# Performance work log

Hardware: AMD Instinct MI355X
Metric: run time of the kernel (lower is better)

## Reference

```python
import jax, jax.numpy as jnp
import numpy as np

B, N, K = 2, 8192, 9
FEAT_C, COST_C, FLOW_C = 128, 64, 3
CH = [128, 128]          # PointConv output channels
MLP = [128, 64]          # pointwise Conv1d channels
WN = 16                  # WeightNet output width
HID = [8, 8]             # WeightNet hidden widths
SLOPE = 0.1              # leaky relu slope
EPS = 1e-5
CLAMP = (-200.0, 200.0)


def setup_inputs() -> dict:
    key = jax.random.key(0)
    ks = iter(jax.random.split(key, 64))
    def nrm(shape, s=0.02):
        return jax.random.normal(next(ks), shape, jnp.float32) * s
    inp = {}
    inp["xyz"] = jax.random.normal(next(ks), (B, N, 3), jnp.float32)
    inp["feats"] = jax.random.normal(next(ks), (B, FEAT_C, N), jnp.float32)
    inp["cost_volume"] = jax.random.normal(next(ks), (B, COST_C, N), jnp.float32)
    inp["flow"] = jax.random.normal(next(ks), (B, FLOW_C, N), jnp.float32)
    last = FEAT_C + COST_C + FLOW_C
    for i, co in enumerate(CH):
        cin = last + 3
        p = f"pc{i}_"
        inp[p + "w1"] = nrm((HID[0], 3)); inp[p + "b1"] = jnp.zeros((HID[0],), jnp.float32)
        inp[p + "w2"] = nrm((HID[1], HID[0])); inp[p + "b2"] = jnp.zeros((HID[1],), jnp.float32)
        inp[p + "w3"] = nrm((WN, HID[1])); inp[p + "b3"] = jnp.zeros((WN,), jnp.float32)
        inp[p + "linW"] = nrm((co, cin * WN)); inp[p + "linb"] = jnp.zeros((co,), jnp.float32)
        last = co
    for i, co in enumerate(MLP):
        inp[f"mlp{i}_W"] = nrm((co, last)); inp[f"mlp{i}_b"] = jnp.zeros((co,), jnp.float32)
        last = co
    inp["fc_W"] = nrm((3, last)); inp["fc_b"] = jnp.zeros((3,), jnp.float32)
    return inp


def _bn(x, axes):
    m = x.mean(axes, keepdims=True)
    v = x.var(axes, keepdims=True)
    return (x - m) / jnp.sqrt(v + EPS)


def _leaky(x):
    return jnp.where(x >= 0, x, SLOPE * x)


def _knn_idx(xyz, k):
    # xyz: [B,N,3] -> idx [B,N,K] of k nearest (incl. self)
    sq = jnp.sum(xyz * xyz, -1)                       # [B,N]
    d = sq[:, :, None] + sq[:, None, :] - 2.0 * jnp.einsum('bnc,bmc->bnm', xyz, xyz)
    return jax.lax.top_k(-d, k)[1]                    # [B,N,K]


def _gather(a, idx):
    # a: [B,N,C], idx: [B,N,K] -> [B,N,K,C]
    return jax.vmap(lambda x, i: x[i])(a, idx)


def _pointconv(xyz, points, idx, w1, b1, w2, b2, w3, b3, linW, linb):
    # xyz [B,N,3], points [B,C,N] -> [B,out,N]
    g_xyz = _gather(xyz, idx) - xyz[:, :, None, :]    # [B,N,K,3] relative coords
    g_pts = _gather(jnp.transpose(points, (0, 2, 1)), idx)  # [B,N,K,C]
    grouped = jnp.concatenate([g_pts, g_xyz], -1)     # [B,N,K,C+3]
    # WeightNet on relative coords: 3 -> 8 -> 8 -> 16 (bn+relu each)
    h = jax.nn.relu(_bn(g_xyz @ w1.T + b1, (0, 1, 2)))
    h = jax.nn.relu(_bn(h @ w2.T + b2, (0, 1, 2)))
    w = jax.nn.relu(_bn(h @ w3.T + b3, (0, 1, 2)))    # [B,N,K,WN]
    bsz, n = grouped.shape[0], grouped.shape[1]
    agg = jnp.einsum('bnkc,bnkw->bncw', grouped, w).reshape(bsz, n, -1)
    out = agg @ linW.T + linb                         # [B,N,out]
    out = _leaky(_bn(out, (0, 1)))
    return jnp.transpose(out, (0, 2, 1))              # [B,out,N]


def reference(xyz, feats, cost_volume, flow,
              pc0_w1, pc0_b1, pc0_w2, pc0_b2, pc0_w3, pc0_b3, pc0_linW, pc0_linb,
              pc1_w1, pc1_b1, pc1_w2, pc1_b2, pc1_w3, pc1_b3, pc1_linW, pc1_linb,
              mlp0_W, mlp0_b, mlp1_W, mlp1_b, fc_W, fc_b):
    idx = _knn_idx(xyz, K)
    x = jnp.concatenate([feats, cost_volume, flow], axis=1)  # [B, feat+cost+flow, N]
    x = _pointconv(xyz, x, idx, pc0_w1, pc0_b1, pc0_w2, pc0_b2, pc0_w3, pc0_b3, pc0_linW, pc0_linb)
    x = _pointconv(xyz, x, idx, pc1_w1, pc1_b1, pc1_w2, pc1_b2, pc1_w3, pc1_b3, pc1_linW, pc1_linb)
    x = _leaky(jnp.einsum('oc,bcn->bon', mlp0_W, x) + mlp0_b[None, :, None])
    x = _leaky(jnp.einsum('oc,bcn->bon', mlp1_W, x) + mlp1_b[None, :, None])
    fl = jnp.einsum('oc,bcn->bon', fc_W, x) + fc_b[None, :, None]
    return x, jnp.clip(fl, CLAMP[0], CLAMP[1])
```

## Files before the change

### kernel.cpp

```cpp
#include <hip/hip_runtime.h>

#define NBATCH 2
#define NPTS   8192
#define NPT    (NBATCH*NPTS)
#define KNN    9
#define SEG    16
#define SEGN   (NPTS/SEG)
#define SCAP   16
#define SSTR   17

typedef unsigned short u16;
typedef unsigned int   u32;
typedef short bf16x8 __attribute__((ext_vector_type(8)));
typedef float f32x4  __attribute__((ext_vector_type(4)));

__device__ __forceinline__ float wred(float v){
#pragma unroll
  for(int o=32;o>0;o>>=1) v += __shfl_down(v,o);
  return v;
}

__device__ __forceinline__ u16 f2b(float f){
  u32 u = __float_as_uint(f);
  return (u16)((u + 0x7fffu + ((u>>16)&1u)) >> 16);
}

__device__ __forceinline__ float bumpup(float x){
  u32 u = __float_as_uint(x);
  if(u == 0x80000000u) u = 1u;
  else if((int)u >= 0) u += 1u;
  else u -= 1u;
  return __uint_as_float(u);
}

__global__ __launch_bounds__(256) void k_build_xin(
    const float* __restrict__ feats, const float* __restrict__ cost,
    const float* __restrict__ flow, float* __restrict__ xin)
{
  __shared__ float buf[196][67];
  int t = threadIdx.x;
  int pt0 = blockIdx.x*64;
  int b = pt0 >> 13, n0 = pt0 & (NPTS-1);
  int lane = t & 63, grp = t >> 6;
  const float* f  = feats + (size_t)b*128*NPTS + n0 + lane;
  const float* cv = cost  + (size_t)b*64 *NPTS + n0 + lane;
  const float* fl = flow  + (size_t)b*3  *NPTS + n0 + lane;
  for(int c=grp; c<128; c+=4) buf[c][lane]      = f[(size_t)c*NPTS];
  for(int c=grp; c<64;  c+=4) buf[128+c][lane]  = cv[(size_t)c*NPTS];
  if(grp<3) buf[192+grp][lane] = fl[(size_t)grp*NPTS];
  else      buf[195][lane] = 0.f;
  __syncthreads();
  for(int e=t; e<64*49; e+=256){
    int p = e/49, q = e-p*49;
    float4 v = make_float4(buf[4*q][p], buf[4*q+1][p], buf[4*q+2][p], buf[4*q+3][p]);
    *(float4*)(xin + (size_t)(pt0+p)*196 + 4*q) = v;
  }
}

__global__ __launch_bounds__(256) void k_thr(
    const float* __restrict__ xyz, float* __restrict__ thr)
{
  __shared__ float md[4][64][9];
  int t = threadIdx.x, lane = t & 63, wave = t >> 6;
  int qb = blockIdx.x;
  int b = qb >> 7;
  int n = (qb & 127)*64 + lane;
  const float* xb = xyz + (size_t)b*NPTS*3;
  float qx=xb[3*n], qy=xb[3*n+1], qz=xb[3*n+2];
  float qs = __fadd_rn(__fadd_rn(__fmul_rn(qx,qx),__fmul_rn(qy,qy)),__fmul_rn(qz,qz));
  float bd[KNN];
#pragma unroll
  for(int i=0;i<KNN;i++) bd[i]=__builtin_inff();
  for(int i=0;i<128;i++){
    int m = (wave*128 + i)*16;
    float cx=xb[3*m], cy=xb[3*m+1], cz=xb[3*m+2];
    float s = __fadd_rn(__fadd_rn(__fmul_rn(cx,cx),__fmul_rn(cy,cy)),__fmul_rn(cz,cz));
    float dot = fmaf(cz,qz, fmaf(cy,qy, __fmul_rn(cx,qx)));
    float d = __fsub_rn(__fadd_rn(qs,s), __fmul_rn(2.0f,dot));
    if(d < bd[KNN-1]){
      bd[KNN-1]=d;
#pragma unroll
      for(int r=KNN-2;r>=0;r--){
        if(bd[r+1] < bd[r]){ float td=bd[r]; bd[r]=bd[r+1]; bd[r+1]=td; }
      }
    }
  }
#pragma unroll
  for(int i=0;i<KNN;i++) md[wave][lane][i]=bd[i];
  __syncthreads();
  if(t < 64){
    float b2[KNN];
#pragma unroll
    for(int i=0;i<KNN;i++) b2[i]=__builtin_inff();
    for(int w=0;w<4;w++){
#pragma unroll
      for(int i=0;i<KNN;i++){
        float d = md[w][t][i];
        if(d < b2[KNN-1]){
          b2[KNN-1]=d;
#pragma unroll
          for(int r=KNN-2;r>=0;r--){
            if(b2[r+1] < b2[r]){ float td=b2[r]; b2[r]=b2[r+1]; b2[r+1]=td; }
          }
        }
      }
    }
    thr[(b<<13) + (qb & 127)*64 + t] = b2[KNN-1];
  }
}

__global__ __launch_bounds__(256) void k_knn_part(
    const float* __restrict__ xyz, const float* __restrict__ thr,
    float* __restrict__ pd, int* __restrict__ pi)
{
  __shared__ float4 cbuf[256];
  __shared__ float sdq[256*SSTR];
  __shared__ int   sqi[256*SSTR];
  int t = threadIdx.x;
  int seg = blockIdx.x & (SEG-1);
  int qc  = blockIdx.x >> 4;
  int b = qc >> 5;
  int n = (qc & 31)*256 + t;
  int pt = (b<<13) + n;
  const float* xb = xyz + (size_t)b*NPTS*3;
  float qx=xb[3*n], qy=xb[3*n+1], qz=xb[3*n+2];
  float qs = __fadd_rn(__fadd_rn(__fmul_rn(qx,qx),__fmul_rn(qy,qy)),__fmul_rn(qz,qz));
  float init = bumpup(thr[pt]);
  float bd[KNN]; int bi[KNN];
#pragma unroll
  for(int i=0;i<KNN;i++){ bd[i]=init; bi[i]=0x7fffffff; }
  float cut = init;
  int cnt = 0;
  float* msd = sdq + t*SSTR;
  int*   msi = sqi + t*SSTR;
  auto flush = [&](){
    for(int i=0;i<cnt;i++){
      float d = msd[i]; int id = msi[i];
      if(d < bd[KNN-1]){
        bd[KNN-1]=d; bi[KNN-1]=id;
#pragma unroll
        for(int r=KNN-2;r>=0;r--){
          if(bd[r+1] < bd[r]){
            float td=bd[r]; bd[r]=bd[r+1]; bd[r+1]=td;
            int ti=bi[r]; bi[r]=bi[r+1]; bi[r+1]=ti;
          }
        }
      }
    }
    cnt = 0;
    cut = bd[KNN-1];
  };
  const int m0 = seg*SEGN;
  for(int tt=0; tt<SEGN; tt+=256){
    int m = m0 + tt + t;
    float cx=xb[3*m], cy=xb[3*m+1], cz=xb[3*m+2];
    float s = __fadd_rn(__fadd_rn(__fmul_rn(cx,cx),__fmul_rn(cy,cy)),__fmul_rn(cz,cz));
    cbuf[t] = make_float4(cx,cy,cz,s);
    __syncthreads();
    for(int j0=0; j0<256; j0+=8){
      float dv[8];
#pragma unroll
      for(int u=0;u<8;u++){
        float4 c = cbuf[j0+u];
        float dot = fmaf(c.z,qz, fmaf(c.y,qy, __fmul_rn(c.x,qx)));
        dv[u] = __fsub_rn(__fadd_rn(qs,c.w), __fmul_rn(2.0f,dot));
      }
#pragma unroll
      for(int u=0;u<8;u++){
        if(dv[u] < cut){
          msd[cnt]=dv[u]; msi[cnt]=m0+tt+j0+u; cnt++;
          if(cnt==SCAP) flush();
        }
      }
    }
    __syncthreads();
  }
  flush();
  size_t base = ((size_t)pt*SEG + seg)*KNN;
#pragma unroll
  for(int i=0;i<KNN;i++){ pd[base+i]=bd[i]; pi[base+i]=bi[i]; }
}

__global__ __launch_bounds__(256) void k_knn_merge(
    const float* __restrict__ pd, const int* __restrict__ pi, int* __restrict__ idxo)
{
  int pt = blockIdx.x*256 + threadIdx.x;
  const float4* dp = (const float4*)(pd + (size_t)pt*SEG*KNN);
  const int4*   ip = (const int4*)(pi + (size_t)pt*SEG*KNN);
  float bd[KNN]; int bi[KNN];
#pragma unroll
  for(int i=0;i<KNN;i++){ bd[i]=__builtin_inff(); bi[i]=0x7fffffff; }
  for(int v=0; v<SEG*KNN/4; v++){
    float4 dv = dp[v];
    int4   iv = ip[v];
    float dd[4] = {dv.x,dv.y,dv.z,dv.w};
    int   ii[4] = {iv.x,iv.y,iv.z,iv.w};
#pragma unroll
    for(int u=0;u<4;u++){
      float d = dd[u]; int id = ii[u];
      if(d < bd[KNN-1]){
        bd[KNN-1]=d; bi[KNN-1]=id;
#pragma unroll
        for(int i=KNN-2;i>=0;i--){
          if(bd[i+1] < bd[i]){
            float td=bd[i]; bd[i]=bd[i+1]; bd[i+1]=td;
            int ti=bi[i]; bi[i]=bi[i+1]; bi[i+1]=ti;
          }
        }
      }
    }
  }
#pragma unroll
  for(int r=0;r<KNN;r++) idxo[pt*KNN + r] = bi[r];
}

__global__ __launch_bounds__(256) void k_wn1(
    const float* __restrict__ xyz, const int* __restrict__ idx,
    const float* __restrict__ W, const float* __restrict__ Bv,
    float* __restrict__ hout, float* __restrict__ partial)
{
  int t = threadIdx.x;
  int e = blockIdx.x*256 + t;
  int pt = e/KNN;
  int b = pt>>13, n = pt & (NPTS-1);
  int m = idx[e];
  const float* xb = xyz + (size_t)b*NPTS*3;
  float gx = xb[3*m]-xb[3*n], gy = xb[3*m+1]-xb[3*n+1], gz = xb[3*m+2]-xb[3*n+2];
  float v[8];
#pragma unroll
  for(int j=0;j<8;j++){
    float d = fmaf(gz, W[3*j+2], fmaf(gy, W[3*j+1], gx*W[3*j]));
    v[j] = d + Bv[j];
    hout[(size_t)e*8 + j] = v[j];
  }
  __shared__ float red[4][2][8];
  int wave = t>>6, lane = t&63;
#pragma unroll
  for(int j=0;j<8;j++){
    float s = wred(v[j]);
    float q = wred(v[j]*v[j]);
    if(lane==0){ red[wave][0][j]=s; red[wave][1][j]=q; }
  }
  __syncthreads();
  if(t < 16){
    int isq = t>>3, c = t&7;
    partial[blockIdx.x*16 + t] =
      red[0][isq][c]+red[1][isq][c]+red[2][isq][c]+red[3][isq][c];
  }
}

template<int CI, int CO>
__global__ __launch_bounds__(256) void k_wn23(
    const float* __restrict__ hin, const float* __restrict__ st,
    const float* __restrict__ W, const float* __restrict__ Bv,
    float* __restrict__ hout, float* __restrict__ partial)
{
  int t = threadIdx.x;
  int e = blockIdx.x*256 + t;
  float x[CI];
#pragma unroll
  for(int i=0;i<CI;i++){
    float v = (hin[(size_t)e*CI + i] - st[i])*st[CI+i];
    x[i] = v>0.f? v : 0.f;
  }
  float v[CO];
#pragma unroll
  for(int j=0;j<CO;j++){
    float d = 0.f;
#pragma unroll
    for(int i=0;i<CI;i++) d = fmaf(x[i], W[j*CI+i], d);
    v[j] = d + Bv[j];
    hout[(size_t)e*CO + j] = v[j];
  }
  __shared__ float red[4][2][CO];
  int wave = t>>6, lane = t&63;
#pragma unroll
  for(int j=0;j<CO;j++){
    float s = wred(v[j]);
    float q = wred(v[j]*v[j]);
    if(lane==0){ red[wave][0][j]=s; red[wave][1][j]=q; }
  }
  __syncthreads();
  if(t < 2*CO){
    int isq = t/CO, c = t%CO;
    partial[blockIdx.x*2*CO + t] =
      red[0][isq][c]+red[1][isq][c]+red[2][isq][c]+red[3][isq][c];
  }
}

__global__ __launch_bounds__(256) void k_fin(
    const float* __restrict__ partial, float* __restrict__ st,
    int C, int nb, float cnt)
{
  __shared__ float sa[256], qa[256];
  int t = threadIdx.x;
  int c = t % C;
  int r0 = t / C;
  int stride = 256 / C;
  float s=0.f, q=0.f;
  for(int r=r0; r<nb; r+=stride){
    s += partial[r*2*C + c];
    q += partial[r*2*C + C + c];
  }
  sa[t]=s; qa[t]=q;
  __syncthreads();
  if(t < C){
    for(int g=1; g<stride; g++){ s += sa[t+g*C]; q += qa[t+g*C]; }
    float mean = s/cnt;
    float var  = q/cnt - mean*mean;
    st[t]   = mean;
    st[C+t] = 1.0f/sqrtf(var + 1e-5f);
  }
}

__global__ __launch_bounds__(256) void k_prepW(
    const float* __restrict__ linW, u16* __restrict__ Wh, int AW, int KP)
{
  int e = blockIdx.x*256 + threadIdx.x;
  if(e >= 128*KP) return;
  int o = e / KP, k = e - o*KP;
  float w = (k < AW) ? linW[o*AW + k] : 0.f;
  Wh[e] = f2b(w);
}

template<int CIN, int XSTRIDE, int KP>
__global__ __launch_bounds__(256) void k_buildA(
    const float* __restrict__ xin, const float* __restrict__ xyz,
    const int* __restrict__ idx, const float* __restrict__ wpre,
    const float* __restrict__ st3, u16* __restrict__ Abuf, int c0)
{
  constexpr int P = 8;
  constexpr int CPTS = CIN-3;
  constexpr int CPAD = KP/16;
  __shared__ float wm[P][KNN][16];
  __shared__ float gxs[P][KNN][3];
  __shared__ int   si[P][KNN];
  __shared__ float sm3[16], sr3[16];
  int t = threadIdx.x;
  int pt0 = c0 + blockIdx.x*P;
  int b = pt0 >> 13;
  const float* xb = xyz + (size_t)b*NPTS*3;
  if(t<16){ sm3[t]=st3[t]; sr3[t]=st3[16+t]; }
  if(t>=32 && t<32+P*KNN){
    int u = t-32; int p=u/KNN, k=u-p*KNN;
    int n = (pt0+p)&(NPTS-1);
    int m = idx[(pt0+p)*KNN+k];
    si[p][k]=m;
    gxs[p][k][0]=xb[3*m]  -xb[3*n];
    gxs[p][k][1]=xb[3*m+1]-xb[3*n+1];
    gxs[p][k][2]=xb[3*m+2]-xb[3*n+2];
  }
  __syncthreads();
  for(int e=t; e<P*KNN*16; e+=256){
    int p = e/(KNN*16); int r = e - p*(KNN*16); int k = r>>4, wn = r&15;
    float v = (wpre[((size_t)(pt0+p)*KNN + k)*16 + wn] - sm3[wn]) * sr3[wn];
    wm[p][k][wn] = v>0.f? v:0.f;
  }
  __syncthreads();
  for(int it=t; it<P*CPAD; it+=256){
    int p = it/CPAD, c = it - p*CPAD;
    u32 u[8];
    if(c < CIN){
      float g[KNN];
      if(c < CPTS){
#pragma unroll
        for(int k=0;k<KNN;k++)
          g[k] = xin[(size_t)((b<<13) + si[p][k])*XSTRIDE + c];
      } else {
        int cc = c - CPTS;
#pragma unroll
        for(int k=0;k<KNN;k++) g[k] = gxs[p][k][cc];
      }
      float a[16];
#pragma unroll
      for(int wn=0; wn<16; wn++){
        float s = 0.f;
#pragma unroll
        for(int k=0;k<KNN;k++) s = fmaf(g[k], wm[p][k][wn], s);
        a[wn] = s;
      }
#pragma unroll
      for(int j=0;j<8;j++)
        u[j] = (u32)f2b(a[2*j]) | ((u32)f2b(a[2*j+1])<<16);
    } else {
#pragma unroll
      for(int j=0;j<8;j++) u[j]=0;
    }
    u32* dst = (u32*)(Abuf + ((size_t)(blockIdx.x*P + p)*KP + c*16));
    uint4 v0 = make_uint4(u[0],u[1],u[2],u[3]);
    uint4 v1 = make_uint4(u[4],u[5],u[6],u[7]);
    *(uint4*)dst = v0;
    *((uint4*)dst + 1) = v1;
  }
}

__device__ __forceinline__ void gload16(const void* g, void* l){
  __builtin_amdgcn_global_load_lds(
      (const __attribute__((address_space(1))) u32*)g,
      (__attribute__((address_space(3))) u32*)l, 16, 0, 0);
}

template<int KP>
__global__ __launch_bounds__(256) void k_gemm(
    const u16* __restrict__ Wh, const u16* __restrict__ A,
    const float* __restrict__ linb, float* __restrict__ outp,
    float* __restrict__ partial, int ptBase)
{
  __shared__ __attribute__((aligned(16))) u16 lds[24576];
  constexpr int NT = KP/64;
  int t = threadIdx.x, wave = t>>6, lane = t&63;
  int p0 = blockIdx.x*64;
  const u16* Ab = A + (size_t)p0*KP;

  auto stage = [&](const u16* __restrict__ g, int k0, int ldsByteOff, int rows){
    int nr = (rows*128) >> 12;
    for(int r=0;r<nr;r++){
      int y  = (r*4 + wave) << 10;
      int yl = y + lane*16;
      int row = yl >> 7;
      int s = (yl >> 4) & 7;
      int c = s ^ (row & 7);
      const u16* src = g + (size_t)row*KP + k0 + c*8;
      gload16(src, (char*)lds + ldsByteOff + y);
    }
  };

  stage(Wh, 0, 0,     128);
  stage(Ab, 0, 32768, 64);

  f32x4 acc[2][4];
#pragma unroll
  for(int i=0;i<2;i++)
#pragma unroll
    for(int j=0;j<4;j++) acc[i][j]=(f32x4)(0.f);

  for(int kt=0; kt<NT; kt++){
    int cur = kt & 1;
    __syncthreads();
    if(kt+1 < NT){
      int nxt = cur^1;
      stage(Wh, (kt+1)*64, nxt*16384,         128);
      stage(Ab, (kt+1)*64, 32768 + nxt*8192,  64);
    }
    const u16* Lw = lds + cur*8192;
    const u16* La = lds + 16384 + cur*4096;
#pragma unroll
    for(int kf=0; kf<2; kf++){
      int cb = kf*4 + (lane>>4);
      bf16x8 af[4];
#pragma unroll
      for(int nf=0; nf<4; nf++){
        int p = nf*16 + (lane&15);
        af[nf] = *(const bf16x8*)(La + p*64 + ((cb ^ (p&7))<<3));
      }
#pragma unroll
      for(int mf=0; mf<2; mf++){
        int row = (wave*2+mf)*16 + (lane&15);
        bf16x8 wh = *(const bf16x8*)(Lw + row*64 + ((cb ^ (row&7))<<3));
#pragma unroll
        for(int nf=0; nf<4; nf++)
          acc[mf][nf] = __builtin_amdgcn_mfma_f32_16x16x32_bf16(wh, af[nf], acc[mf][nf], 0,0,0);
      }
    }
  }

  int gb = (ptBase>>6) + blockIdx.x;
  int q = lane>>4, lc = lane&15;
#pragma unroll
  for(int mf=0; mf<2; mf++){
    int obase = (wave*2+mf)*16 + q*4;
#pragma unroll
    for(int r=0;r<4;r++){
      int o = obase + r;
      float bo = linb[o];
      float sv = 0.f, qv = 0.f;
#pragma unroll
      for(int nf=0; nf<4; nf++){
        float x = acc[mf][nf][r] + bo;
        outp[(size_t)(ptBase + p0 + nf*16 + lc)*128 + o] = x;
        sv += x; qv = fmaf(x,x,qv);
      }
#pragma unroll
      for(int off=8; off>0; off>>=1){
        sv += __shfl_down(sv,off);
        qv += __shfl_down(qv,off);
      }
      if(lc==0){
        partial[gb*256 + o]       = sv;
        partial[gb*256 + 128 + o] = qv;
      }
    }
  }
}

__global__ __launch_bounds__(256) void k_pfin(
    const float* __restrict__ outp, const float* __restrict__ st,
    float* __restrict__ xout)
{
  int e = blockIdx.x*256 + threadIdx.x;
  int c = e & 127;
  float v = (outp[e]-st[c])*st[128+c];
  xout[e] = v>=0.f? v : 0.1f*v;
}

__global__ __launch_bounds__(256) void k_mlp(
    const float* __restrict__ x2,
    const float* __restrict__ W0, const float* __restrict__ B0,
    const float* __restrict__ W1, const float* __restrict__ B1,
    const float* __restrict__ Wf, const float* __restrict__ Bf,
    float* __restrict__ dout)
{
  __shared__ float w0l[128*129];
  __shared__ float w1l[128*65];
  __shared__ float xt [128*65];
  __shared__ float m1l[64*65];
  int t = threadIdx.x;
  int pt0 = blockIdx.x*64;
  int b = pt0 >> 13, n0 = pt0 & (NPTS-1);
  for(int e=t; e<128*128; e+=256){ int o=e>>7, j=e&127; w0l[j*129+o] = W0[e]; }
  for(int e=t; e<64*128;  e+=256){ int o=e>>7, j=e&127; w1l[j*65+o]  = W1[e]; }
  for(int e=t; e<64*128;  e+=256){ int p=e>>7, j=e&127; xt[j*65+p]   = x2[(size_t)(pt0+p)*128 + j]; }
  __syncthreads();
  int p = t&63, wv = t>>6;
  float acc[32];
#pragma unroll
  for(int i=0;i<32;i++) acc[i]=0.f;
  for(int j=0;j<128;j++){
    float xv = xt[j*65+p];
#pragma unroll
    for(int i=0;i<32;i++)
      acc[i] = fmaf(w0l[j*129 + wv*32 + i], xv, acc[i]);
  }
  __syncthreads();
#pragma unroll
  for(int i=0;i<32;i++){
    float v = acc[i] + B0[wv*32+i];
    v = v>=0.f? v : 0.1f*v;
    xt[(wv*32+i)*65 + p] = v;
  }
  __syncthreads();
  float a2[16];
#pragma unroll
  for(int i=0;i<16;i++) a2[i]=0.f;
  for(int j=0;j<128;j++){
    float xv = xt[j*65+p];
#pragma unroll
    for(int i=0;i<16;i++)
      a2[i] = fmaf(w1l[j*65 + wv*16 + i], xv, a2[i]);
  }
#pragma unroll
  for(int i=0;i<16;i++){
    int o = wv*16+i;
    float v = a2[i] + B1[o];
    v = v>=0.f? v : 0.1f*v;
    dout[(size_t)(b*64+o)*NPTS + n0 + p] = v;
    m1l[o*65+p] = v;
  }
  __syncthreads();
  if(t < 192){
    int o = t/64, pp = t%64;
    float a = Bf[o];
    for(int j=0;j<64;j++) a = fmaf(Wf[o*64+j], m1l[j*65+pp], a);
    a = fminf(fmaxf(a, -200.f), 200.f);
    dout[(size_t)NBATCH*64*NPTS + (size_t)(b*3+o)*NPTS + n0 + pp] = a;
  }
}

extern "C" void kernel_launch(void* const* d_in, const int* in_sizes, int n_in,
                              void* d_out, int out_size, void* d_ws, size_t ws_size,
                              hipStream_t stream)
{
  (void)in_sizes; (void)n_in; (void)out_size;
  const float* xyz   = (const float*)d_in[0];
  const float* feats = (const float*)d_in[1];
  const float* cost  = (const float*)d_in[2];
  const float* flow  = (const float*)d_in[3];
  const float* pw1[2]  = {(const float*)d_in[4],  (const float*)d_in[12]};
  const float* pb1[2]  = {(const float*)d_in[5],  (const float*)d_in[13]};
  const float* pw2[2]  = {(const float*)d_in[6],  (const float*)d_in[14]};
  const float* pb2[2]  = {(const float*)d_in[7],  (const float*)d_in[15]};
  const float* pw3[2]  = {(const float*)d_in[8],  (const float*)d_in[16]};
  const float* pb3[2]  = {(const float*)d_in[9],  (const float*)d_in[17]};
  const float* plW[2]  = {(const float*)d_in[10], (const float*)d_in[18]};
  const float* plb[2]  = {(const float*)d_in[11], (const float*)d_in[19]};
  const float* m0W = (const float*)d_in[20];
  const float* m0b = (const float*)d_in[21];
  const float* m1W = (const float*)d_in[22];
  const float* m1b = (const float*)d_in[23];
  const float* fcW = (const float*)d_in[24];
  const float* fcb = (const float*)d_in[25];
  float* out = (float*)d_out;

  const int KP0 = 3200, AW0 = 3168;
  const int KP1 = 2112, AW1 = 2096;

  float* ws = (float*)d_ws;
  size_t o = 0;
  float* xin0 = ws + o; o += (size_t)NPT*196;
  int*   idx  = (int*)(ws + o); o += (size_t)NPT*KNN + 3;
  o &= ~(size_t)3;
  float* thr  = ws + o; o += (size_t)NPT;
  float* pd   = ws + o; o += (size_t)NPT*SEG*KNN;
  int*   pi   = (int*)(ws + o); o += (size_t)NPT*SEG*KNN;
  float* h1   = ws + o; o += (size_t)NPT*KNN*8;
  float* h2   = ws + o; o += (size_t)NPT*KNN*8;
  float* wpre = ws + o; o += (size_t)NPT*KNN*16;
  float* part = ws + o; o += 65536;
  float* st1  = ws + o; o += 16;
  float* st2  = ws + o; o += 16;
  float* st3  = ws + o; o += 32;
  float* sto  = ws + o; o += 256;
  float* outp = ws + o; o += (size_t)NPT*128;
  float* x1   = ws + o; o += (size_t)NPT*128;
  float* x2   = ws + o; o += (size_t)NPT*128;
  u16* Wh0 = (u16*)(ws + o); o += (size_t)128*KP0/2;
  u16* Wh1 = (u16*)(ws + o); o += (size_t)128*KP1/2;
  u16* Abuf = (u16*)(ws + o);
  size_t used_bytes = o*4;
  size_t avail = ws_size > used_bytes ? ws_size - used_bytes : 0;
  int npc = NPT;
  while(npc > 1024 && (size_t)npc*KP0*2 > avail) npc >>= 1;

  k_build_xin<<<NPT/64, 256, 0, stream>>>(feats, cost, flow, xin0);
  k_thr<<<256, 256, 0, stream>>>(xyz, thr);
  k_knn_part<<<64*SEG, 256, 0, stream>>>(xyz, thr, pd, pi);
  k_knn_merge<<<NPT/256, 256, 0, stream>>>(pd, pi, idx);

  k_prepW<<<(128*KP0+255)/256, 256, 0, stream>>>(plW[0], Wh0, AW0, KP0);
  k_prepW<<<(128*KP1+255)/256, 256, 0, stream>>>(plW[1], Wh1, AW1, KP1);

  const float cnt1 = (float)(NPT*KNN);
  const float cnto = (float)NPT;

  for(int L=0; L<2; ++L){
    k_wn1<<<576,256,0,stream>>>(xyz, idx, pw1[L], pb1[L], h1, part);
    k_fin<<<1,256,0,stream>>>(part, st1, 8, 576, cnt1);
    k_wn23<8,8><<<576,256,0,stream>>>(h1, st1, pw2[L], pb2[L], h2, part);
    k_fin<<<1,256,0,stream>>>(part, st2, 8, 576, cnt1);
    k_wn23<8,16><<<576,256,0,stream>>>(h2, st2, pw3[L], pb3[L], wpre, part);
    k_fin<<<1,256,0,stream>>>(part, st3, 16, 576, cnt1);
    for(int c0 = 0; c0 < NPT; c0 += npc){
      if(L==0){
        k_buildA<198,196,KP0><<<npc/8,256,0,stream>>>(xin0, xyz, idx, wpre, st3, Abuf, c0);
        k_gemm<KP0><<<npc/64,256,0,stream>>>(Wh0, Abuf, plb[0], outp, part, c0);
      } else {
        k_buildA<131,128,KP1><<<npc/8,256,0,stream>>>(x1, xyz, idx, wpre, st3, Abuf, c0);
        k_gemm<KP1><<<npc/64,256,0,stream>>>(Wh1, Abuf, plb[1], outp, part, c0);
      }
    }
    k_fin<<<1,256,0,stream>>>(part, sto, 128, NPT/64, cnto);
    k_pfin<<<NPT*128/256,256,0,stream>>>(outp, sto, (L==0)? x1 : x2);
  }

  k_mlp<<<NPT/64,256,0,stream>>>(x2, m0W,m0b, m1W,m1b, fcW,fcb, out);
}
```

Before: 567.4 us.

## Fuse BN stat finalization into WeightNet kernels and widen gemm/mlp blocks

Each k_wn23 block now reduces the previous layer's partial sums itself. This removes two single-block k_fin launches per PointConv layer, and each stage gets its own partial buffer. The GEMM kernel moves to 512 threads, with each wave owning one 16-row output fragment instead of two. buildA handles 16 points per block, and the MLP kernel uses 512 threads with fewer accumulators per thread. The aim is less launch overhead and more parallelism per CU, paid for by redundant per-block stat reductions and less register reuse per wave.

```diff
diff --git a/kernel.cpp b/kernel.cpp
--- a/kernel.cpp
+++ b/kernel.cpp
@@ -251,16 +251,39 @@
 
 template<int CI, int CO>
 __global__ __launch_bounds__(256) void k_wn23(
-    const float* __restrict__ hin, const float* __restrict__ st,
+    const float* __restrict__ hin, const float* __restrict__ partialIn,
+    int nb, float cnt,
     const float* __restrict__ W, const float* __restrict__ Bv,
-    float* __restrict__ hout, float* __restrict__ partial)
-{
+    float* __restrict__ hout, float* __restrict__ partialOut)
+{
+  __shared__ float sa[256], qa[256];
+  __shared__ float stl[2*CI];
   int t = threadIdx.x;
+  {
+    int c = t % CI;
+    int r0 = t / CI;
+    int stride = 256 / CI;
+    float s=0.f, q=0.f;
+    for(int r=r0; r<nb; r+=stride){
+      s += partialIn[r*2*CI + c];
+      q += partialIn[r*2*CI + CI + c];
+    }
+    sa[t]=s; qa[t]=q;
+    __syncthreads();
+    if(t < CI){
+      for(int g=1; g<stride; g++){ s += sa[t+g*CI]; q += qa[t+g*CI]; }
+      float mean = s/cnt;
+      float var  = q/cnt - mean*mean;
+      stl[t]    = mean;
+      stl[CI+t] = 1.0f/sqrtf(var + 1e-5f);
+    }
+    __syncthreads();
+  }
   int e = blockIdx.x*256 + t;
   float x[CI];
 #pragma unroll
   for(int i=0;i<CI;i++){
-    float v = (hin[(size_t)e*CI + i] - st[i])*st[CI+i];
+    float v = (hin[(size_t)e*CI + i] - stl[i])*stl[CI+i];
     x[i] = v>0.f? v : 0.f;
   }
   float v[CO];
@@ -283,7 +306,7 @@
   __syncthreads();
   if(t < 2*CO){
     int isq = t/CO, c = t%CO;
-    partial[blockIdx.x*2*CO + t] =
+    partialOut[blockIdx.x*2*CO + t] =
       red[0][isq][c]+red[1][isq][c]+red[2][isq][c]+red[3][isq][c];
   }
 }
@@ -329,7 +352,7 @@
     const int* __restrict__ idx, const float* __restrict__ wpre,
     const float* __restrict__ st3, u16* __restrict__ Abuf, int c0)
 {
-  constexpr int P = 8;
+  constexpr int P = 16;
   constexpr int CPTS = CIN-3;
   constexpr int CPAD = KP/16;
   __shared__ float wm[P][KNN][16];
@@ -341,8 +364,8 @@
   int b = pt0 >> 13;
   const float* xb = xyz + (size_t)b*NPTS*3;
   if(t<16){ sm3[t]=st3[t]; sr3[t]=st3[16+t]; }
-  if(t>=32 && t<32+P*KNN){
-    int u = t-32; int p=u/KNN, k=u-p*KNN;
+  for(int e=t; e<P*KNN; e+=256){
+    int p = e/KNN, k = e - p*KNN;
     int n = (pt0+p)&(NPTS-1);
     int m = idx[(pt0+p)*KNN+k];
     si[p][k]=m;
@@ -401,7 +424,7 @@
 }
 
 template<int KP>
-__global__ __launch_bounds__(256) void k_gemm(
+__global__ __launch_bounds__(512) void k_gemm(
     const u16* __restrict__ Wh, const u16* __restrict__ A,
     const float* __restrict__ linb, float* __restrict__ outp,
     float* __restrict__ partial, int ptBase)
@@ -413,9 +436,9 @@
   const u16* Ab = A + (size_t)p0*KP;
 
   auto stage = [&](const u16* __restrict__ g, int k0, int ldsByteOff, int rows){
-    int nr = (rows*128) >> 12;
+    int nr = (rows*128) >> 13;
     for(int r=0;r<nr;r++){
-      int y  = (r*4 + wave) << 10;
+      int y  = (r*8 + wave) << 10;
       int yl = y + lane*16;
       int row = yl >> 7;
       int s = (yl >> 4) & 7;
@@ -428,11 +451,9 @@
   stage(Wh, 0, 0,     128);
   stage(Ab, 0, 32768, 64);
 
-  f32x4 acc[2][4];
-#pragma unroll
-  for(int i=0;i<2;i++)
-#pragma unroll
-    for(int j=0;j<4;j++) acc[i][j]=(f32x4)(0.f);
+  f32x4 acc[4];
+#pragma unroll
+  for(int j=0;j<4;j++) acc[j]=(f32x4)(0.f);
 
   for(int kt=0; kt<NT; kt++){
     int cur = kt & 1;
@@ -453,42 +474,36 @@
         int p = nf*16 + (lane&15);
         af[nf] = *(const bf16x8*)(La + p*64 + ((cb ^ (p&7))<<3));
       }
-#pragma unroll
-      for(int mf=0; mf<2; mf++){
-        int row = (wave*2+mf)*16 + (lane&15);
-        bf16x8 wh = *(const bf16x8*)(Lw + row*64 + ((cb ^ (row&7))<<3));
-#pragma unroll
-        for(int nf=0; nf<4; nf++)
-          acc[mf][nf] = __builtin_amdgcn_mfma_f32_16x16x32_bf16(wh, af[nf], acc[mf][nf], 0,0,0);
-      }
+      int row = wave*16 + (lane&15);
+      bf16x8 wh = *(const bf16x8*)(Lw + row*64 + ((cb ^ (row&7))<<3));
+#pragma unroll
+      for(int nf=0; nf<4; nf++)
+        acc[nf] = __builtin_amdgcn_mfma_f32_16x16x32_bf16(wh, af[nf], acc[nf], 0,0,0);
     }
   }
 
   int gb = (ptBase>>6) + blockIdx.x;
   int q = lane>>4, lc = lane&15;
-#pragma unroll
-  for(int mf=0; mf<2; mf++){
-    int obase = (wave*2+mf)*16 + q*4;
-#pragma unroll
-    for(int r=0;r<4;r++){
-      int o = obase + r;
-      float bo = linb[o];
-      float sv = 0.f, qv = 0.f;
-#pragma unroll
-      for(int nf=0; nf<4; nf++){
-        float x = acc[mf][nf][r] + bo;
-        outp[(size_t)(ptBase + p0 + nf*16 + lc)*128 + o] = x;
-        sv += x; qv = fmaf(x,x,qv);
-      }
-#pragma unroll
-      for(int off=8; off>0; off>>=1){
-        sv += __shfl_down(sv,off);
-        qv += __shfl_down(qv,off);
-      }
-      if(lc==0){
-        partial[gb*256 + o]       = sv;
-        partial[gb*256 + 128 + o] = qv;
-      }
+  int obase = wave*16 + q*4;
+#pragma unroll
+  for(int r=0;r<4;r++){
+    int o = obase + r;
+    float bo = linb[o];
+    float sv = 0.f, qv = 0.f;
+#pragma unroll
+    for(int nf=0; nf<4; nf++){
+      float x = acc[nf][r] + bo;
+      outp[(size_t)(ptBase + p0 + nf*16 + lc)*128 + o] = x;
+      sv += x; qv = fmaf(x,x,qv);
+    }
+#pragma unroll
+    for(int off=8; off>0; off>>=1){
+      sv += __shfl_down(sv,off);
+      qv += __shfl_down(qv,off);
+    }
+    if(lc==0){
+      partial[gb*256 + o]       = sv;
+      partial[gb*256 + 128 + o] = qv;
     }
   }
 }
@@ -503,7 +518,7 @@
   xout[e] = v>=0.f? v : 0.1f*v;
 }
 
-__global__ __launch_bounds__(256) void k_mlp(
+__global__ __launch_bounds__(512) void k_mlp(
     const float* __restrict__ x2,
     const float* __restrict__ W0, const float* __restrict__ B0,
     const float* __restrict__ W1, const float* __restrict__ B1,
@@ -517,40 +532,41 @@
   int t = threadIdx.x;
   int pt0 = blockIdx.x*64;
   int b = pt0 >> 13, n0 = pt0 & (NPTS-1);
-  for(int e=t; e<128*128; e+=256){ int o=e>>7, j=e&127; w0l[j*129+o] = W0[e]; }
-  for(int e=t; e<64*128;  e+=256){ int o=e>>7, j=e&127; w1l[j*65+o]  = W1[e]; }
-  for(int e=t; e<64*128;  e+=256){ int p=e>>7, j=e&127; xt[j*65+p]   = x2[(size_t)(pt0+p)*128 + j]; }
+  for(int e=t; e<128*128; e+=512){ int o=e>>7, j=e&127; w0l[j*129+o] = W0[e]; }
+  for(int e=t; e<64*128;  e+=512){ int o=e>>7, j=e&127; w1l[j*65+o]  = W1[e]; }
+  for(int e=t; e<64*128;  e+=512){ int p=e>>7, j=e&127; xt[j*65+p]   = x2[(size_t)(pt0+p)*128 + j]; }
   __syncthreads();
   int p = t&63, wv = t>>6;
-  float acc[32];
-#pragma unroll
-  for(int i=0;i<32;i++) acc[i]=0.f;
+  float acc[16];
+#pragma unroll
+  for(int i=0;i<16;i++) acc[i]=0.f;
   for(int j=0;j<128;j++){
     float xv = xt[j*65+p];
 #pragma unroll
-    for(int i=0;i<32;i++)
-      acc[i] = fmaf(w0l[j*129 + wv*32 + i], xv, acc[i]);
-  }
-  __syncthreads();
-#pragma unroll
-  for(int i=0;i<32;i++){
-    float v = acc[i] + B0[wv*32+i];
+    for(int i=0;i<16;i++)
+      acc[i] = fmaf(w0l[j*129 + wv*16 + i], xv, acc[i]);
+  }
+  __syncthreads();
+#pragma unroll
+  for(int i=0;i<16;i++){
+    int o = wv*16+i;
+    float v = acc[i] + B0[o];
     v = v>=0.f? v : 0.1f*v;
-    xt[(wv*32+i)*65 + p] = v;
-  }
-  __syncthreads();
-  float a2[16];
-#pragma unroll
-  for(int i=0;i<16;i++) a2[i]=0.f;
+    xt[o*65 + p] = v;
+  }
+  __syncthreads();
+  float a2[8];
+#pragma unroll
+  for(int i=0;i<8;i++) a2[i]=0.f;
   for(int j=0;j<128;j++){
     float xv = xt[j*65+p];
 #pragma unroll
-    for(int i=0;i<16;i++)
-      a2[i] = fmaf(w1l[j*65 + wv*16 + i], xv, a2[i]);
-  }
-#pragma unroll
-  for(int i=0;i<16;i++){
-    int o = wv*16+i;
+    for(int i=0;i<8;i++)
+      a2[i] = fmaf(w1l[j*65 + wv*8 + i], xv, a2[i]);
+  }
+#pragma unroll
+  for(int i=0;i<8;i++){
+    int o = wv*8+i;
     float v = a2[i] + B1[o];
     v = v>=0.f? v : 0.1f*v;
     dout[(size_t)(b*64+o)*NPTS + n0 + p] = v;
@@ -605,9 +621,10 @@
   float* h1   = ws + o; o += (size_t)NPT*KNN*8;
   float* h2   = ws + o; o += (size_t)NPT*KNN*8;
   float* wpre = ws + o; o += (size_t)NPT*KNN*16;
-  float* part = ws + o; o += 65536;
-  float* st1  = ws + o; o += 16;
-  float* st2  = ws + o; o += 16;
+  float* part1 = ws + o; o += 576*16;
+  float* part2 = ws + o; o += 576*16;
+  float* part3 = ws + o; o += 576*32;
+  float* parto = ws + o; o += 65536;
   float* st3  = ws + o; o += 32;
   float* sto  = ws + o; o += 256;
   float* outp = ws + o; o += (size_t)NPT*128;
@@ -633,24 +650,22 @@
   const float cnto = (float)NPT;
 
   for(int L=0; L<2; ++L){
-    k_wn1<<<576,256,0,stream>>>(xyz, idx, pw1[L], pb1[L], h1, part);
-    k_fin<<<1,256,0,stream>>>(part, st1, 8, 576, cnt1);
-    k_wn23<8,8><<<576,256,0,stream>>>(h1, st1, pw2[L], pb2[L], h2, part);
-    k_fin<<<1,256,0,stream>>>(part, st2, 8, 576, cnt1);
-    k_wn23<8,16><<<576,256,0,stream>>>(h2, st2, pw3[L], pb3[L], wpre, part);
-    k_fin<<<1,256,0,stream>>>(part, st3, 16, 576, cnt1);
+    k_wn1<<<576,256,0,stream>>>(xyz, idx, pw1[L], pb1[L], h1, part1);
+    k_wn23<8,8><<<576,256,0,stream>>>(h1, part1, 576, cnt1, pw2[L], pb2[L], h2, part2);
+    k_wn23<8,16><<<576,256,0,stream>>>(h2, part2, 576, cnt1, pw3[L], pb3[L], wpre, part3);
+    k_fin<<<1,256,0,stream>>>(part3, st3, 16, 576, cnt1);
     for(int c0 = 0; c0 < NPT; c0 += npc){
       if(L==0){
-        k_buildA<198,196,KP0><<<npc/8,256,0,stream>>>(xin0, xyz, idx, wpre, st3, Abuf, c0);
-        k_gemm<KP0><<<npc/64,256,0,stream>>>(Wh0, Abuf, plb[0], outp, part, c0);
+        k_buildA<198,196,KP0><<<npc/16,256,0,stream>>>(xin0, xyz, idx, wpre, st3, Abuf, c0);
+        k_gemm<KP0><<<npc/64,512,0,stream>>>(Wh0, Abuf, plb[0], outp, parto, c0);
       } else {
-        k_buildA<131,128,KP1><<<npc/8,256,0,stream>>>(x1, xyz, idx, wpre, st3, Abuf, c0);
-        k_gemm<KP1><<<npc/64,256,0,stream>>>(Wh1, Abuf, plb[1], outp, part, c0);
-      }
-    }
-    k_fin<<<1,256,0,stream>>>(part, sto, 128, NPT/64, cnto);
+        k_buildA<131,128,KP1><<<npc/16,256,0,stream>>>(x1, xyz, idx, wpre, st3, Abuf, c0);
+        k_gemm<KP1><<<npc/64,512,0,stream>>>(Wh1, Abuf, plb[1], outp, parto, c0);
+      }
+    }
+    k_fin<<<1,256,0,stream>>>(parto, sto, 128, NPT/64, cnto);
     k_pfin<<<NPT*128/256,256,0,stream>>>(outp, sto, (L==0)? x1 : x2);
   }
 
-  k_mlp<<<NPT/64,256,0,stream>>>(x2, m0W,m0b, m1W,m1b, fcW,fcb, out);
-}
+  k_mlp<<<NPT/64,512,0,stream>>>(x2, m0W,m0b, m1W,m1b, fcW,fcb, out);
+}
```

New measurement: 561.2 us. About the same (-1.1%).
